# Performance work log

Hardware: AMD Instinct MI355X
Metric: run time of the kernel (lower is better)

## Reference

```python
import jax, jax.numpy as jnp
import numpy as np

B, F, T, D, O = 8192, 512, 64, 6, 128
N_INTERNAL = 2 ** D - 1  # 63
N_LEAVES = 2 ** D        # 64


def smooth_step(t):
    tc = jnp.clip(t, -0.5, 0.5)
    return -2.0 * tc ** 3 + 1.5 * tc + 0.5


def setup_inputs() -> dict:
    key = jax.random.key(0)
    k1, k2, k3, k4 = jax.random.split(key, 4)
    x = jax.random.normal(k1, (B, F), dtype=jnp.float32)
    # Stacked per-node Linear weights in BFS (heap) order: node i -> row i.
    W_nodes = jax.random.normal(k2, (N_INTERNAL, F, T), dtype=jnp.float32) * (1.0 / np.sqrt(F))
    b_nodes = jax.random.normal(k3, (N_INTERNAL, T), dtype=jnp.float32) * 0.01
    # Per-leaf mixing weight [out_features, num_trees], leaves in BFS order.
    W_leaf = jax.random.normal(k4, (N_LEAVES, O, T), dtype=jnp.float32)
    return {"x": x, "W_nodes": W_nodes, "b_nodes": b_nodes, "W_leaf": W_leaf}


def reference(x, W_nodes, b_nodes, W_leaf):
    n_internal = W_nodes.shape[0]
    depth = int(np.log2(n_internal + 1))
    # All internal-node gates in one stacked GEMM: [B, n_internal, T]
    s = smooth_step(jnp.einsum('bf,nft->bnt', x, W_nodes) + b_nodes[None, :, :])
    b, _, t = s.shape
    prob = jnp.ones((b, 1, t), dtype=s.dtype)  # root prob
    start = 0
    for lvl in range(depth):
        width = 2 ** lvl
        s_l = s[:, start:start + width]  # [B, width, T], nodes at this level
        start += width
        # node local j -> children local 2j (left, prob*s) and 2j+1 (right, prob*(1-s))
        prob = jnp.stack([prob * s_l, prob * (1.0 - s_l)], axis=2).reshape(b, 2 * width, t)
    # prob: [B, n_leaves, T]; mix per-leaf, per-tree weights -> [B, O]
    out = jnp.einsum('blt,lot->bo', prob, W_leaf)
    return out
```

## Files before the change

kernel.cpp:

```cpp
#include <hip/hip_runtime.h>
#include <hip/hip_fp16.h>

#define BATCH 8192
#define FDIM  512
#define NTREE 64
#define NODES 63
#define ODIM  128
#define NJP   4096
#define K2    4096
#define KS    8

typedef _Float16 f16;
typedef _Float16 f16x2 __attribute__((ext_vector_type(2)));
typedef _Float16 f16x8 __attribute__((ext_vector_type(8)));
typedef float    f32x4 __attribute__((ext_vector_type(4)));

#define XH_OFF   0
#define XH_SZ    ((size_t)BATCH*FDIM*2)
#define WNH_OFF  (XH_OFF + XH_SZ)
#define WNH_SZ   ((size_t)NJP*FDIM*2)
#define WLT_OFF  (WNH_OFF + WNH_SZ)
#define WLT_SZ   ((size_t)ODIM*K2*2)
#define SP_OFF   (WLT_OFF + WLT_SZ)
#define SP_SZ    ((size_t)BATCH*NJP*2)
#define PS_OFF   (SP_OFF + SP_SZ)
#define PS_SZ    ((size_t)KS*BATCH*ODIM*4)
#define WS_MIN   (SP_OFF + SP_SZ)
#define WS_FULL  (PS_OFF + PS_SZ)

__device__ __forceinline__ float smooth_step_f(float t) {
    float tc = fminf(fmaxf(t, -0.5f), 0.5f);
    return fmaf(tc, fmaf(-2.0f * tc, tc, 1.5f), 0.5f);
}

__device__ __forceinline__ void async16(const void* g, void* l) {
    __builtin_amdgcn_global_load_lds((__attribute__((address_space(1))) void*)g,
                                     (__attribute__((address_space(3))) void*)l,
                                     16, 0, 0);
}

__device__ __forceinline__ int sw_off(int row, int g) {
    return ((row >> 3) * 512) + (((row & 7) * 8 + (g ^ (row & 7))) * 8);
}

__global__ void conv_x_kernel(const float* __restrict__ in, f16* __restrict__ out) {
    size_t i = ((size_t)blockIdx.x * blockDim.x + threadIdx.x) * 4;
    float4 v = *(const float4*)(in + i);
    f16* o = out + i;
    o[0] = (f16)v.x; o[1] = (f16)v.y; o[2] = (f16)v.z; o[3] = (f16)v.w;
}

__global__ void conv_wl_kernel(const float* __restrict__ in, f16* __restrict__ out) {
    __shared__ f16 tile[64][72];
    const int o    = blockIdx.x;
    const int lane = threadIdx.x & 63;
    const int w    = threadIdx.x >> 6;
    #pragma unroll
    for (int lc = 0; lc < 16; ++lc) {
        int l = w * 16 + lc;
        tile[lane][l] = (f16)in[(size_t)l * (ODIM * NTREE) + o * 64 + lane];
    }
    __syncthreads();
    f16* orow = out + (size_t)o * K2;
    #pragma unroll
    for (int c = 0; c < 2; ++c) {
        int idx = (threadIdx.x * 2 + c) * 8;
        int t = idx >> 6, l = idx & 63;
        f16x8 v;
        #pragma unroll
        for (int e = 0; e < 8; ++e) v[e] = tile[t][l + e];
        *(f16x8*)(orow + idx) = v;
    }
}

__global__ void conv_wn_kernel(const float* __restrict__ wn, f16* __restrict__ out) {
    const int n    = blockIdx.x;
    const int f0   = blockIdx.y * 64;
    const int lane = threadIdx.x & 63;
    const int w    = threadIdx.x >> 6;
    if (n == NODES) {
        #pragma unroll
        for (int tc = 0; tc < 16; ++tc) {
            int t = w * 16 + tc;
            out[(size_t)(t * 64 + NODES) * FDIM + f0 + lane] = (f16)0.0f;
        }
        return;
    }
    __shared__ float tile[64][65];
    const float* src = wn + (size_t)n * (FDIM * NTREE);
    #pragma unroll
    for (int i = 0; i < 16; ++i) {
        int fl = w * 16 + i;
        tile[fl][lane] = src[(size_t)(f0 + fl) * NTREE + lane];
    }
    __syncthreads();
    #pragma unroll
    for (int i = 0; i < 16; ++i) {
        int t = w * 16 + i;
        out[(size_t)(t * 64 + n) * FDIM + f0 + lane] = (f16)tile[lane][t];
    }
}

__global__ __launch_bounds__(256, 3)
void gemm_nodes(const f16* __restrict__ xh, const f16* __restrict__ wnh,
                const float* __restrict__ bn, f16* __restrict__ prob_out)
{
    __shared__ f16 SH[128 * 130];
    f16* Ash = SH;
    f16* Bsh = SH + 128 * 64;
    const int tid  = threadIdx.x;
    const int lane = tid & 63;
    const int w    = tid >> 6;
    const int wm   = w & 1;
    const int wn   = w >> 1;
    const int j0   = blockIdx.x * 128;
    const int row0 = blockIdx.y * 128;

    const int lr = lane >> 3;
    const int lg = (lane & 7) ^ lr;
    f32x4 acc[4][4] = {};

    for (int k0 = 0; k0 < FDIM; k0 += 64) {
        #pragma unroll
        for (int q = 0; q < 8; ++q) {
            int id = w * 8 + q;
            if (id < 16) {
                int r = id * 8 + lr;
                async16(xh + (size_t)(row0 + r) * FDIM + k0 + lg * 8, &Ash[id * 512 + lane * 8]);
            } else {
                int c = id - 16;
                int r = c * 8 + lr;
                async16(wnh + (size_t)(j0 + r) * FDIM + k0 + lg * 8, &Bsh[c * 512 + lane * 8]);
            }
        }
        __syncthreads();
        #pragma unroll
        for (int ks = 0; ks < 2; ++ks) {
            int g = ks * 4 + (lane >> 4);
            f16x8 bfr[4];
            #pragma unroll
            for (int tn = 0; tn < 4; ++tn) {
                int j = wn * 64 + tn * 16 + (lane & 15);
                bfr[tn] = *(const f16x8*)&Bsh[sw_off(j, g)];
            }
            #pragma unroll
            for (int tm = 0; tm < 4; ++tm) {
                int m = wm * 64 + tm * 16 + (lane & 15);
                f16x8 afr = *(const f16x8*)&Ash[sw_off(m, g)];
                #pragma unroll
                for (int tn = 0; tn < 4; ++tn)
                    acc[tm][tn] = __builtin_amdgcn_mfma_f32_16x16x32_f16(afr, bfr[tn], acc[tm][tn], 0, 0, 0);
            }
        }
        __syncthreads();
    }

    #pragma unroll
    for (int tn = 0; tn < 4; ++tn) {
        int col = wn * 64 + tn * 16 + (lane & 15);
        int c   = j0 + col;
        int nn  = c & 63, tt = c >> 6;
        float bias = (nn < NODES) ? bn[nn * NTREE + tt] : 0.0f;
        #pragma unroll
        for (int tm = 0; tm < 4; ++tm) {
            #pragma unroll
            for (int r = 0; r < 4; ++r) {
                int row = wm * 64 + tm * 16 + (lane >> 4) * 4 + r;
                SH[row * 130 + col] = (f16)smooth_step_f(acc[tm][tn][r] + bias);
            }
        }
    }
    __syncthreads();

    {
        const int row = tid & 127;
        const int tr  = tid >> 7;
        const f16* gp = &SH[row * 130 + tr * 64];

        float g[64];
        #pragma unroll
        for (int c = 0; c < 32; ++c) {
            f16x2 v = *(const f16x2*)(gp + 2 * c);
            g[2 * c]     = (float)v[0];
            g[2 * c + 1] = (float)v[1];
        }

        float pr[32];
        pr[0] = 1.0f;
        int bse = 0;
        #pragma unroll
        for (int lvl = 0; lvl < 5; ++lvl) {
            const int width = 1 << lvl;
            #pragma unroll
            for (int i = width - 1; i >= 0; --i) {
                float p = pr[i], s = g[bse + i];
                pr[2 * i]     = p * s;
                pr[2 * i + 1] = p * (1.0f - s);
            }
            bse += width;
        }
        f16x8 ov[8];
        #pragma unroll
        for (int i = 0; i < 32; ++i) {
            float s5 = g[31 + i];
            float p  = pr[i];
            ov[i >> 2][(i & 3) * 2]     = (f16)(p * s5);
            ov[i >> 2][(i & 3) * 2 + 1] = (f16)(p * (1.0f - s5));
        }
        f16* dst = prob_out + (size_t)(row0 + row) * NJP + (size_t)(blockIdx.x * 2 + tr) * 64;
        #pragma unroll
        for (int c = 0; c < 8; ++c) ((f16x8*)dst)[c] = ov[c];
    }
}

__global__ __launch_bounds__(256, 4)
void leaf_gemm(const f16* __restrict__ prob, const f16* __restrict__ wlt,
               float* __restrict__ out, float* __restrict__ partial)
{
    __shared__ f16 SH[128 * 128];
    f16* Ash = SH;
    f16* Bsh = SH + 128 * 64;
    const int tid  = threadIdx.x;
    const int lane = tid & 63;
    const int w    = tid >> 6;
    const int wm   = w & 1;
    const int wn   = w >> 1;
    const int row0 = blockIdx.x * 128;
    const int nks  = gridDim.y;
    const int kch  = K2 / nks;
    const int kbeg = blockIdx.y * kch;
    float* dst = (nks == 1) ? out : partial + (size_t)blockIdx.y * BATCH * ODIM;

    const int lr = lane >> 3;
    const int lg = (lane & 7) ^ lr;
    f32x4 acc[4][4] = {};

    for (int k0 = kbeg; k0 < kbeg + kch; k0 += 64) {
        #pragma unroll
        for (int q = 0; q < 8; ++q) {
            int id = w * 8 + q;
            if (id < 16) {
                int r = id * 8 + lr;
                async16(prob + (size_t)(row0 + r) * NJP + k0 + lg * 8, &Ash[id * 512 + lane * 8]);
            } else {
                int c = id - 16;
                int o = c * 8 + lr;
                async16(wlt + (size_t)o * K2 + k0 + lg * 8, &Bsh[c * 512 + lane * 8]);
            }
        }
        __syncthreads();
        #pragma unroll
        for (int ks = 0; ks < 2; ++ks) {
            int g = ks * 4 + (lane >> 4);
            f16x8 bfr[4];
            #pragma unroll
            for (int tn = 0; tn < 4; ++tn) {
                int o = wn * 64 + tn * 16 + (lane & 15);
                bfr[tn] = *(const f16x8*)&Bsh[sw_off(o, g)];
            }
            #pragma unroll
            for (int tm = 0; tm < 4; ++tm) {
                int m = wm * 64 + tm * 16 + (lane & 15);
                f16x8 afr = *(const f16x8*)&Ash[sw_off(m, g)];
                #pragma unroll
                for (int tn = 0; tn < 4; ++tn)
                    acc[tm][tn] = __builtin_amdgcn_mfma_f32_16x16x32_f16(afr, bfr[tn], acc[tm][tn], 0, 0, 0);
            }
        }
        __syncthreads();
    }
    #pragma unroll
    for (int tn = 0; tn < 4; ++tn) {
        int o = wn * 64 + tn * 16 + (lane & 15);
        #pragma unroll
        for (int tm = 0; tm < 4; ++tm) {
            #pragma unroll
            for (int r = 0; r < 4; ++r) {
                int row = row0 + wm * 64 + tm * 16 + (lane >> 4) * 4 + r;
                dst[(size_t)row * ODIM + o] = acc[tm][tn][r];
            }
        }
    }
}

__global__ void reduce_kernel(const float* __restrict__ partial, float* __restrict__ out) {
    size_t i = ((size_t)blockIdx.x * blockDim.x + threadIdx.x) * 4;
    f32x4 a = *(const f32x4*)(partial + i);
    #pragma unroll
    for (int k = 1; k < KS; ++k)
        a += *(const f32x4*)(partial + (size_t)k * BATCH * ODIM + i);
    *(f32x4*)(out + i) = a;
}

#define ROWS 8
__global__ __launch_bounds__(256, 2)
void soft_tree_fallback(const float* __restrict__ x, const float* __restrict__ Wn,
                        const float* __restrict__ bn, const float* __restrict__ Wl,
                        float* __restrict__ out)
{
    __shared__ __half s_lds[ROWS][NODES][NTREE];
    const int lane = threadIdx.x & 63;
    const int w    = threadIdx.x >> 6;
    const long row0 = (long)blockIdx.x * ROWS;
    for (int n = w; n < NODES; n += 4) {
        const float* wp = Wn + ((long)n * FDIM) * NTREE + lane;
        const float* xp = x + row0 * FDIM;
        float acc[ROWS];
        #pragma unroll
        for (int r = 0; r < ROWS; ++r) acc[r] = 0.0f;
        #pragma unroll 8
        for (int f = 0; f < FDIM; ++f) {
            float wv = wp[(long)f * NTREE];
            #pragma unroll
            for (int r = 0; r < ROWS; ++r)
                acc[r] = fmaf(xp[r * FDIM + f], wv, acc[r]);
        }
        float bias = bn[n * NTREE + lane];
        #pragma unroll
        for (int r = 0; r < ROWS; ++r)
            s_lds[r][n][lane] = __float2half(smooth_step_f(acc[r] + bias));
    }
    __syncthreads();
    const int r0 = w * 2, r1 = w * 2 + 1;
    float pr0[64], pr1[64];
    {
        pr0[0] = 1.0f; pr1[0] = 1.0f;
        int base = 0;
        #pragma unroll
        for (int lvl = 0; lvl < 6; ++lvl) {
            const int width = 1 << lvl;
            #pragma unroll
            for (int i = width - 1; i >= 0; --i) {
                float sa = __half2float(s_lds[r0][base + i][lane]);
                float sb = __half2float(s_lds[r1][base + i][lane]);
                float pa = pr0[i], pb = pr1[i];
                pr0[2 * i] = pa * sa; pr0[2 * i + 1] = pa * (1.0f - sa);
                pr1[2 * i] = pb * sb; pr1[2 * i + 1] = pb * (1.0f - sb);
            }
            base += width;
        }
    }
    for (int o = 0; o < ODIM; ++o) {
        const float* wlp = Wl + (long)o * NTREE + lane;
        float c0 = 0.0f, c1 = 0.0f;
        #pragma unroll
        for (int l = 0; l < 64; ++l) {
            float wv = wlp[(long)l * (ODIM * NTREE)];
            c0 = fmaf(pr0[l], wv, c0);
            c1 = fmaf(pr1[l], wv, c1);
        }
        #pragma unroll
        for (int off = 32; off > 0; off >>= 1) {
            c0 += __shfl_xor(c0, off, 64);
            c1 += __shfl_xor(c1, off, 64);
        }
        if (lane == 0) {
            out[(row0 + r0) * ODIM + o] = c0;
            out[(row0 + r1) * ODIM + o] = c1;
        }
    }
}

extern "C" void kernel_launch(void* const* d_in, const int* in_sizes, int n_in,
                              void* d_out, int out_size, void* d_ws, size_t ws_size,
                              hipStream_t stream) {
    const float* x  = (const float*)d_in[0];
    const float* Wn = (const float*)d_in[1];
    const float* bn = (const float*)d_in[2];
    const float* Wl = (const float*)d_in[3];
    float* out = (float*)d_out;

    if (ws_size < WS_MIN) {
        soft_tree_fallback<<<BATCH / ROWS, 256, 0, stream>>>(x, Wn, bn, Wl, out);
        return;
    }

    f16*   xh  = (f16*)((char*)d_ws + XH_OFF);
    f16*   wnh = (f16*)((char*)d_ws + WNH_OFF);
    f16*   wlt = (f16*)((char*)d_ws + WLT_OFF);
    f16*   sp  = (f16*)((char*)d_ws + SP_OFF);
    float* ps  = (float*)((char*)d_ws + PS_OFF);

    conv_x_kernel <<<(BATCH * FDIM) / (256 * 4), 256, 0, stream>>>(x, xh);
    conv_wl_kernel<<<ODIM, 256, 0, stream>>>(Wl, wlt);
    conv_wn_kernel<<<dim3(64, FDIM / 64), 256, 0, stream>>>(Wn, wnh);

    gemm_nodes<<<dim3(NJP / 128, BATCH / 128), 256, 0, stream>>>(xh, wnh, bn, sp);

    if (ws_size >= WS_FULL) {
        leaf_gemm<<<dim3(BATCH / 128, KS), 256, 0, stream>>>(sp, wlt, out, ps);
        reduce_kernel<<<(BATCH * ODIM) / (256 * 4), 256, 0, stream>>>(ps, out);
    } else {
        leaf_gemm<<<dim3(BATCH / 128, 1), 256, 0, stream>>>(sp, wlt, out, nullptr);
    }
}
```

Before: 176.8 us.

## Fuse node GEMM, tree probability expansion and leaf GEMM into one kernel

Merges the gate GEMM and the leaf-mixing GEMM into a single kernel. Each block computes 128 rows by 128 node-tree columns of gates, expands them into leaf probabilities in LDS, and accumulates them directly into the leaf output across four tree-pair chunks. This stops writing and reading the 64 MB fp16 probability matrix through global memory. The cost is a larger LDS footprint, lower occupancy (launch bounds 2 instead of 3/4), and more serialized work per block, since each block runs four node GEMMs plus the leaf MFMAs without overlap.

```diff
diff --git a/kernel.cpp b/kernel.cpp
--- a/kernel.cpp
+++ b/kernel.cpp
@@ -8,7 +8,7 @@
 #define ODIM  128
 #define NJP   4096
 #define K2    4096
-#define KS    8
+#define TPG   8
 
 typedef _Float16 f16;
 typedef _Float16 f16x2 __attribute__((ext_vector_type(2)));
@@ -21,12 +21,9 @@
 #define WNH_SZ   ((size_t)NJP*FDIM*2)
 #define WLT_OFF  (WNH_OFF + WNH_SZ)
 #define WLT_SZ   ((size_t)ODIM*K2*2)
-#define SP_OFF   (WLT_OFF + WLT_SZ)
-#define SP_SZ    ((size_t)BATCH*NJP*2)
-#define PS_OFF   (SP_OFF + SP_SZ)
-#define PS_SZ    ((size_t)KS*BATCH*ODIM*4)
-#define WS_MIN   (SP_OFF + SP_SZ)
-#define WS_FULL  (PS_OFF + PS_SZ)
+#define PS_OFF   (WLT_OFF + WLT_SZ)
+#define PS_SZ    ((size_t)TPG*BATCH*ODIM*4)
+#define WS_NEEDED (PS_OFF + PS_SZ)
 
 __device__ __forceinline__ float smooth_step_f(float t) {
     float tc = fminf(fmaxf(t, -0.5f), 0.5f);
@@ -101,174 +98,156 @@
     }
 }
 
-__global__ __launch_bounds__(256, 3)
-void gemm_nodes(const f16* __restrict__ xh, const f16* __restrict__ wnh,
-                const float* __restrict__ bn, f16* __restrict__ prob_out)
+__global__ __launch_bounds__(256, 2)
+void fused_tree(const f16* __restrict__ xh, const f16* __restrict__ wnh,
+                const float* __restrict__ bn, const f16* __restrict__ wlt,
+                float* __restrict__ partial)
 {
-    __shared__ f16 SH[128 * 130];
-    f16* Ash = SH;
-    f16* Bsh = SH + 128 * 64;
-    const int tid  = threadIdx.x;
-    const int lane = tid & 63;
-    const int w    = tid >> 6;
-    const int wm   = w & 1;
-    const int wn   = w >> 1;
-    const int j0   = blockIdx.x * 128;
-    const int row0 = blockIdx.y * 128;
-
-    const int lr = lane >> 3;
-    const int lg = (lane & 7) ^ lr;
-    f32x4 acc[4][4] = {};
-
-    for (int k0 = 0; k0 < FDIM; k0 += 64) {
-        #pragma unroll
-        for (int q = 0; q < 8; ++q) {
-            int id = w * 8 + q;
-            if (id < 16) {
-                int r = id * 8 + lr;
-                async16(xh + (size_t)(row0 + r) * FDIM + k0 + lg * 8, &Ash[id * 512 + lane * 8]);
-            } else {
-                int c = id - 16;
-                int r = c * 8 + lr;
-                async16(wnh + (size_t)(j0 + r) * FDIM + k0 + lg * 8, &Bsh[c * 512 + lane * 8]);
-            }
-        }
-        __syncthreads();
-        #pragma unroll
-        for (int ks = 0; ks < 2; ++ks) {
-            int g = ks * 4 + (lane >> 4);
-            f16x8 bfr[4];
-            #pragma unroll
-            for (int tn = 0; tn < 4; ++tn) {
-                int j = wn * 64 + tn * 16 + (lane & 15);
-                bfr[tn] = *(const f16x8*)&Bsh[sw_off(j, g)];
-            }
-            #pragma unroll
-            for (int tm = 0; tm < 4; ++tm) {
-                int m = wm * 64 + tm * 16 + (lane & 15);
-                f16x8 afr = *(const f16x8*)&Ash[sw_off(m, g)];
-                #pragma unroll
-                for (int tn = 0; tn < 4; ++tn)
-                    acc[tm][tn] = __builtin_amdgcn_mfma_f32_16x16x32_f16(afr, bfr[tn], acc[tm][tn], 0, 0, 0);
-            }
-        }
-        __syncthreads();
-    }
-
-    #pragma unroll
-    for (int tn = 0; tn < 4; ++tn) {
-        int col = wn * 64 + tn * 16 + (lane & 15);
-        int c   = j0 + col;
-        int nn  = c & 63, tt = c >> 6;
-        float bias = (nn < NODES) ? bn[nn * NTREE + tt] : 0.0f;
-        #pragma unroll
-        for (int tm = 0; tm < 4; ++tm) {
-            #pragma unroll
-            for (int r = 0; r < 4; ++r) {
-                int row = wm * 64 + tm * 16 + (lane >> 4) * 4 + r;
-                SH[row * 130 + col] = (f16)smooth_step_f(acc[tm][tn][r] + bias);
-            }
-        }
-    }
-    __syncthreads();
-
-    {
-        const int row = tid & 127;
-        const int tr  = tid >> 7;
-        const f16* gp = &SH[row * 130 + tr * 64];
-
-        float g[64];
-        #pragma unroll
-        for (int c = 0; c < 32; ++c) {
-            f16x2 v = *(const f16x2*)(gp + 2 * c);
-            g[2 * c]     = (float)v[0];
-            g[2 * c + 1] = (float)v[1];
-        }
-
-        float pr[32];
-        pr[0] = 1.0f;
-        int bse = 0;
-        #pragma unroll
-        for (int lvl = 0; lvl < 5; ++lvl) {
-            const int width = 1 << lvl;
-            #pragma unroll
-            for (int i = width - 1; i >= 0; --i) {
-                float p = pr[i], s = g[bse + i];
-                pr[2 * i]     = p * s;
-                pr[2 * i + 1] = p * (1.0f - s);
-            }
-            bse += width;
-        }
-        f16x8 ov[8];
-        #pragma unroll
-        for (int i = 0; i < 32; ++i) {
-            float s5 = g[31 + i];
-            float p  = pr[i];
-            ov[i >> 2][(i & 3) * 2]     = (f16)(p * s5);
-            ov[i >> 2][(i & 3) * 2 + 1] = (f16)(p * (1.0f - s5));
-        }
-        f16* dst = prob_out + (size_t)(row0 + row) * NJP + (size_t)(blockIdx.x * 2 + tr) * 64;
-        #pragma unroll
-        for (int c = 0; c < 8; ++c) ((f16x8*)dst)[c] = ov[c];
-    }
-}
-
-__global__ __launch_bounds__(256, 4)
-void leaf_gemm(const f16* __restrict__ prob, const f16* __restrict__ wlt,
-               float* __restrict__ out, float* __restrict__ partial)
-{
-    __shared__ f16 SH[128 * 128];
-    f16* Ash = SH;
-    f16* Bsh = SH + 128 * 64;
+    __shared__ f16 SH[33024];
+    f16* CT = SH + 16384;
     const int tid  = threadIdx.x;
     const int lane = tid & 63;
     const int w    = tid >> 6;
     const int wm   = w & 1;
     const int wn   = w >> 1;
     const int row0 = blockIdx.x * 128;
-    const int nks  = gridDim.y;
-    const int kch  = K2 / nks;
-    const int kbeg = blockIdx.y * kch;
-    float* dst = (nks == 1) ? out : partial + (size_t)blockIdx.y * BATCH * ODIM;
+    const int tpg  = blockIdx.y;
 
     const int lr = lane >> 3;
     const int lg = (lane & 7) ^ lr;
-    f32x4 acc[4][4] = {};
-
-    for (int k0 = kbeg; k0 < kbeg + kch; k0 += 64) {
+    const int frow = tid & 127;
+    const int ftr  = tid >> 7;
+
+    f32x4 lacc[4][4] = {};
+
+    for (int tpi = 0; tpi < 4; ++tpi) {
+        const int tp = tpg * 4 + tpi;
+        const int j0 = tp * 128;
+
+        f32x4 acc[4][4] = {};
+        for (int k0 = 0; k0 < FDIM; k0 += 64) {
+            #pragma unroll
+            for (int q = 0; q < 8; ++q) {
+                int id = w * 8 + q;
+                if (id < 16) {
+                    int r = id * 8 + lr;
+                    async16(xh + (size_t)(row0 + r) * FDIM + k0 + lg * 8, &SH[id * 512 + lane * 8]);
+                } else {
+                    int c = id - 16;
+                    int r = c * 8 + lr;
+                    async16(wnh + (size_t)(j0 + r) * FDIM + k0 + lg * 8, &SH[8192 + c * 512 + lane * 8]);
+                }
+            }
+            __syncthreads();
+            #pragma unroll
+            for (int ks = 0; ks < 2; ++ks) {
+                int g = ks * 4 + (lane >> 4);
+                f16x8 bfr[4];
+                #pragma unroll
+                for (int tn = 0; tn < 4; ++tn) {
+                    int j = wn * 64 + tn * 16 + (lane & 15);
+                    bfr[tn] = *(const f16x8*)&SH[8192 + sw_off(j, g)];
+                }
+                #pragma unroll
+                for (int tm = 0; tm < 4; ++tm) {
+                    int m = wm * 64 + tm * 16 + (lane & 15);
+                    f16x8 afr = *(const f16x8*)&SH[sw_off(m, g)];
+                    #pragma unroll
+                    for (int tn = 0; tn < 4; ++tn)
+                        acc[tm][tn] = __builtin_amdgcn_mfma_f32_16x16x32_f16(afr, bfr[tn], acc[tm][tn], 0, 0, 0);
+                }
+            }
+            __syncthreads();
+        }
+
         #pragma unroll
         for (int q = 0; q < 8; ++q) {
             int id = w * 8 + q;
-            if (id < 16) {
-                int r = id * 8 + lr;
-                async16(prob + (size_t)(row0 + r) * NJP + k0 + lg * 8, &Ash[id * 512 + lane * 8]);
-            } else {
-                int c = id - 16;
-                int o = c * 8 + lr;
-                async16(wlt + (size_t)o * K2 + k0 + lg * 8, &Bsh[c * 512 + lane * 8]);
+            int h = id >> 4, c = id & 15;
+            int o = c * 8 + lr;
+            async16(wlt + (size_t)o * K2 + j0 + h * 64 + lg * 8,
+                    &SH[h * 8192 + c * 512 + lane * 8]);
+        }
+
+        #pragma unroll
+        for (int tn = 0; tn < 4; ++tn) {
+            int col = wn * 64 + tn * 16 + (lane & 15);
+            int nn  = col & 63;
+            int tt  = (j0 + col) >> 6;
+            float bias = (nn < NODES) ? bn[nn * NTREE + tt] : 0.0f;
+            #pragma unroll
+            for (int tm = 0; tm < 4; ++tm) {
+                #pragma unroll
+                for (int r = 0; r < 4; ++r) {
+                    int row = wm * 64 + tm * 16 + (lane >> 4) * 4 + r;
+                    CT[row * 130 + col] = (f16)smooth_step_f(acc[tm][tn][r] + bias);
+                }
             }
         }
         __syncthreads();
-        #pragma unroll
-        for (int ks = 0; ks < 2; ++ks) {
-            int g = ks * 4 + (lane >> 4);
+
+        f16x8 ov[8];
+        {
+            const f16* gp = &CT[frow * 130 + ftr * 64];
+            float g[64];
+            #pragma unroll
+            for (int c = 0; c < 32; ++c) {
+                f16x2 v = *(const f16x2*)(gp + 2 * c);
+                g[2 * c]     = (float)v[0];
+                g[2 * c + 1] = (float)v[1];
+            }
+            float pr[32];
+            pr[0] = 1.0f;
+            int bse = 0;
+            #pragma unroll
+            for (int lvl = 0; lvl < 5; ++lvl) {
+                const int width = 1 << lvl;
+                #pragma unroll
+                for (int i = width - 1; i >= 0; --i) {
+                    float p = pr[i], s = g[bse + i];
+                    pr[2 * i]     = p * s;
+                    pr[2 * i + 1] = p * (1.0f - s);
+                }
+                bse += width;
+            }
+            #pragma unroll
+            for (int i = 0; i < 32; ++i) {
+                float s5 = g[31 + i];
+                float p  = pr[i];
+                ov[i >> 2][(i & 3) * 2]     = (f16)(p * s5);
+                ov[i >> 2][(i & 3) * 2 + 1] = (f16)(p * (1.0f - s5));
+            }
+        }
+        __syncthreads();
+
+        #pragma unroll
+        for (int g2 = 0; g2 < 8; ++g2)
+            *(f16x8*)&SH[16384 + ftr * 8192 + sw_off(frow, g2)] = ov[g2];
+        __syncthreads();
+
+        #pragma unroll
+        for (int ks2 = 0; ks2 < 4; ++ks2) {
+            int h  = ks2 >> 1;
+            int gg = (ks2 & 1) * 4 + (lane >> 4);
             f16x8 bfr[4];
             #pragma unroll
             for (int tn = 0; tn < 4; ++tn) {
                 int o = wn * 64 + tn * 16 + (lane & 15);
-                bfr[tn] = *(const f16x8*)&Bsh[sw_off(o, g)];
+                bfr[tn] = *(const f16x8*)&SH[h * 8192 + sw_off(o, gg)];
             }
             #pragma unroll
             for (int tm = 0; tm < 4; ++tm) {
                 int m = wm * 64 + tm * 16 + (lane & 15);
-                f16x8 afr = *(const f16x8*)&Ash[sw_off(m, g)];
+                f16x8 afr = *(const f16x8*)&SH[16384 + h * 8192 + sw_off(m, gg)];
                 #pragma unroll
                 for (int tn = 0; tn < 4; ++tn)
-                    acc[tm][tn] = __builtin_amdgcn_mfma_f32_16x16x32_f16(afr, bfr[tn], acc[tm][tn], 0, 0, 0);
+                    lacc[tm][tn] = __builtin_amdgcn_mfma_f32_16x16x32_f16(afr, bfr[tn], lacc[tm][tn], 0, 0, 0);
             }
         }
         __syncthreads();
     }
+
+    float* dst = partial + (size_t)tpg * BATCH * ODIM;
     #pragma unroll
     for (int tn = 0; tn < 4; ++tn) {
         int o = wn * 64 + tn * 16 + (lane & 15);
@@ -277,7 +256,7 @@
             #pragma unroll
             for (int r = 0; r < 4; ++r) {
                 int row = row0 + wm * 64 + tm * 16 + (lane >> 4) * 4 + r;
-                dst[(size_t)row * ODIM + o] = acc[tm][tn][r];
+                dst[(size_t)row * ODIM + o] = lacc[tm][tn][r];
             }
         }
     }
@@ -287,7 +266,7 @@
     size_t i = ((size_t)blockIdx.x * blockDim.x + threadIdx.x) * 4;
     f32x4 a = *(const f32x4*)(partial + i);
     #pragma unroll
-    for (int k = 1; k < KS; ++k)
+    for (int k = 1; k < TPG; ++k)
         a += *(const f32x4*)(partial + (size_t)k * BATCH * ODIM + i);
     *(f32x4*)(out + i) = a;
 }
@@ -370,7 +349,7 @@
     const float* Wl = (const float*)d_in[3];
     float* out = (float*)d_out;
 
-    if (ws_size < WS_MIN) {
+    if (ws_size < WS_NEEDED) {
         soft_tree_fallback<<<BATCH / ROWS, 256, 0, stream>>>(x, Wn, bn, Wl, out);
         return;
     }
@@ -378,19 +357,12 @@
     f16*   xh  = (f16*)((char*)d_ws + XH_OFF);
     f16*   wnh = (f16*)((char*)d_ws + WNH_OFF);
     f16*   wlt = (f16*)((char*)d_ws + WLT_OFF);
-    f16*   sp  = (f16*)((char*)d_ws + SP_OFF);
     float* ps  = (float*)((char*)d_ws + PS_OFF);
 
     conv_x_kernel <<<(BATCH * FDIM) / (256 * 4), 256, 0, stream>>>(x, xh);
     conv_wl_kernel<<<ODIM, 256, 0, stream>>>(Wl, wlt);
     conv_wn_kernel<<<dim3(64, FDIM / 64), 256, 0, stream>>>(Wn, wnh);
 
-    gemm_nodes<<<dim3(NJP / 128, BATCH / 128), 256, 0, stream>>>(xh, wnh, bn, sp);
-
-    if (ws_size >= WS_FULL) {
-        leaf_gemm<<<dim3(BATCH / 128, KS), 256, 0, stream>>>(sp, wlt, out, ps);
-        reduce_kernel<<<(BATCH * ODIM) / (256 * 4), 256, 0, stream>>>(ps, out);
-    } else {
-        leaf_gemm<<<dim3(BATCH / 128, 1), 256, 0, stream>>>(sp, wlt, out, nullptr);
-    }
-}
+    fused_tree<<<dim3(BATCH / 128, TPG), 256, 0, stream>>>(xh, wnh, bn, wlt, ps);
+    reduce_kernel<<<(BATCH * ODIM) / (256 * 4), 256, 0, stream>>>(ps, out);
+}
```

After: 160.1 us. 9.4% less time.
